# Performance work log

Measured on AMD Instinct MI355X. Metric: run time of the kernel, lower is better.

Reference implementation:

```python
import jax, jax.numpy as jnp
import numpy as np

EPS = 1e-5


def setup_inputs() -> dict:
    key = jax.random.key(0)
    ks = jax.random.split(key, 8)
    b, n, l, e = 2, 16, 1024, 512
    qd, kd, vd = 64, 64, 64
    x = jax.random.normal(ks[0], (b, n, l, e), dtype=jnp.float32)
    past_kv = jax.random.normal(ks[1], (b, n, kd, vd), dtype=jnp.float32)
    s = 1.0 / np.sqrt(e)
    Wq = jax.random.normal(ks[2], (qd, e), dtype=jnp.float32) * s
    bq = jnp.zeros((qd,), dtype=jnp.float32)
    Wk = jax.random.normal(ks[3], (kd, e), dtype=jnp.float32) * s
    bk = jnp.zeros((kd,), dtype=jnp.float32)
    Wv = jax.random.normal(ks[4], (vd, e), dtype=jnp.float32) * s
    bv = jnp.zeros((vd,), dtype=jnp.float32)
    return {"x": x, "past_kv": past_kv, "Wq": Wq, "bq": bq,
            "Wk": Wk, "bk": bk, "Wv": Wv, "bv": bv}


def reference(x, past_kv, Wq, bq, Wk, bk, Wv, bv):
    b, n, l, e = x.shape
    # QKV projections on the last axis: [b,n,l,e] -> [b,n,l,d]
    q = jnp.einsum('bnle,de->bnld', x, Wq) + bq
    k = jnp.einsum('bnle,de->bnld', x, Wk) + bk
    v = jnp.einsum('bnle,de->bnld', x, Wv) + bv
    # RetNet per-head decay: 1 - 2^(-5-h), shape [1,n,1,1,1]
    decay = 1.0 - jnp.exp2(-5.0 - jnp.arange(n, dtype=jnp.float32))
    decay = decay.reshape(1, n, 1, 1, 1)
    # decayed state + per-position outer product k_t (x) v_t -> [b,n,l,kd,vd]
    current_kv = decay * past_kv[:, :, None, :, :] + k[..., :, None] * v[..., None, :]
    # Q-weighted reduction over k_dim -> [b,n,l,vd]
    out = jnp.einsum('bnlk,bnlkv->bnlv', q, current_kv)
    # F.group_norm(out, num_groups=n): per (b, head), normalize over (l, vd)
    mean = jnp.mean(out, axis=(2, 3), keepdims=True)
    var = jnp.var(out, axis=(2, 3), keepdims=True)
    out = (out - mean) * jax.lax.rsqrt(var + EPS)
    return out, current_kv
```

## Files before the change

### kernel.cpp

```cpp
#include <hip/hip_runtime.h>


constexpr int B  = 2;
constexpr int NH = 16;
constexpr int L  = 1024;
constexpr int E  = 512;
constexpr int D  = 64;
constexpr int M  = B * NH * L;
constexpr int NQKV = 192;
constexpr int BLK = 32;
constexpr int NBLKS = M / BLK;
constexpr float EPS = 1e-5f;

using short8 = __attribute__((ext_vector_type(8))) short;
using f32x4  = __attribute__((ext_vector_type(4))) float;

__device__ __forceinline__ unsigned short f2bf(float f) {
    union { float f; unsigned int u; } x; x.f = f;
    unsigned int u = x.u;
    return (unsigned short)((u + 0x7fffu + ((u >> 16) & 1u)) >> 16);
}
__device__ __forceinline__ float bf2f(unsigned short h) {
    union { unsigned int u; float f; } x; x.u = ((unsigned int)h) << 16;
    return x.f;
}

__global__ __launch_bounds__(256) void convw_kernel(
    const float* __restrict__ Wq, const float* __restrict__ Wk,
    const float* __restrict__ Wv, unsigned short* __restrict__ Wb)
{
    int idx = blockIdx.x * 256 + threadIdx.x;
    const float* src = (idx < 8192) ? Wq : (idx < 16384) ? Wk : Wv;
    int off = idx & 8191;
    float4 v = ((const float4*)src)[off];
    Wb[(size_t)idx * 4 + 0] = f2bf(v.x);
    Wb[(size_t)idx * 4 + 1] = f2bf(v.y);
    Wb[(size_t)idx * 4 + 2] = f2bf(v.z);
    Wb[(size_t)idx * 4 + 3] = f2bf(v.w);
}

__global__ __launch_bounds__(512) void proj_mfma_kernel(
    const float* __restrict__ x, const unsigned short* __restrict__ Wb,
    const float* __restrict__ bq, const float* __restrict__ bk,
    const float* __restrict__ bv,
    unsigned short* __restrict__ qkvb)
{
    constexpr int BM = 64, BK = 64, LDP = 72;
    __shared__ unsigned short Xs[BM][LDP];
    __shared__ unsigned short Ws[NQKV][LDP];
    __shared__ float bias_s[NQKV];

    const int tid  = threadIdx.x;
    const int row0 = blockIdx.x * BM;
    if (tid < NQKV)
        bias_s[tid] = (tid < 64) ? bq[tid] : (tid < 128) ? bk[tid - 64] : bv[tid - 128];

    const int wid  = tid >> 6;
    const int lane = tid & 63;
    const int wr   = wid >> 2;
    const int wc   = wid & 3;
    const int l15  = lane & 15;
    const int lk   = (lane >> 4) * 8;

    f32x4 acc[2][3] = {};

    for (int k0 = 0; k0 < E; k0 += BK) {
        float4 xa[2];
        #pragma unroll
        for (int j = 0; j < 2; ++j) {
            int f = tid + j * 512;
            xa[j] = *(const float4*)&x[(size_t)(row0 + (f >> 4)) * E + k0 + (f & 15) * 4];
        }
        short8 wch[3];
        #pragma unroll
        for (int j = 0; j < 3; ++j) {
            int c = tid + j * 512;
            wch[j] = *(const short8*)&Wb[(size_t)(c >> 3) * E + k0 + (c & 7) * 8];
        }
        __syncthreads();
        #pragma unroll
        for (int j = 0; j < 2; ++j) {
            int f = tid + j * 512;
            unsigned short t4[4] = {f2bf(xa[j].x), f2bf(xa[j].y),
                                    f2bf(xa[j].z), f2bf(xa[j].w)};
            *(uint2*)&Xs[f >> 4][(f & 15) * 4] = *(uint2*)t4;
        }
        #pragma unroll
        for (int j = 0; j < 3; ++j) {
            int c = tid + j * 512;
            *(short8*)&Ws[c >> 3][(c & 7) * 8] = wch[j];
        }
        __syncthreads();

        #pragma unroll
        for (int kk = 0; kk < 2; ++kk) {
            short8 a[2], b[3];
            #pragma unroll
            for (int mi = 0; mi < 2; ++mi)
                a[mi] = *(const short8*)&Xs[wr * 32 + mi * 16 + l15][kk * 32 + lk];
            #pragma unroll
            for (int ni = 0; ni < 3; ++ni)
                b[ni] = *(const short8*)&Ws[wc * 48 + ni * 16 + l15][kk * 32 + lk];
            #pragma unroll
            for (int mi = 0; mi < 2; ++mi)
                #pragma unroll
                for (int ni = 0; ni < 3; ++ni)
                    acc[mi][ni] = __builtin_amdgcn_mfma_f32_16x16x32_bf16(
                        a[mi], b[ni], acc[mi][ni], 0, 0, 0);
        }
    }

    #pragma unroll
    for (int mi = 0; mi < 2; ++mi) {
        #pragma unroll
        for (int ni = 0; ni < 3; ++ni) {
            int col = wc * 48 + ni * 16 + l15;
            float bb = bias_s[col];
            #pragma unroll
            for (int j = 0; j < 4; ++j) {
                int row = wr * 32 + mi * 16 + (lane >> 4) * 4 + j;
                qkvb[(size_t)(row0 + row) * NQKV + col] = f2bf(acc[mi][ni][j] + bb);
            }
        }
    }
}

__global__ __launch_bounds__(512) void retention_kernel(
    const unsigned short* __restrict__ qkvb,
    const float* __restrict__ past_kv,
    float* __restrict__ out_pre,
    float* __restrict__ ckv,
    float* __restrict__ partials)
{
    const int blk  = blockIdx.x;
    const int bn   = blk >> 5;
    const int pos0 = (blk & 31) * BLK;
    const int h    = bn & (NH - 1);
    const int tid  = threadIdx.x;
    const float decay = 1.0f - exp2f(-5.0f - (float)h);

    __shared__ float pkv_s[64 * 64];
    __shared__ unsigned short qkv_s[BLK * NQKV];
    __shared__ float qk_s[BLK];
    __shared__ float red[16];

    const float* pkv = past_kv + (size_t)bn * 4096;
    float4 p4[2];
    #pragma unroll
    for (int j = 0; j < 2; ++j) {
        p4[j] = *(const float4*)&pkv[(tid + j * 512) * 4];
        *(float4*)&pkv_s[(tid + j * 512) * 4] = p4[j];
    }
    const unsigned short* qrow = qkvb + (size_t)(bn * L + pos0) * NQKV;
    for (int f = tid; f < 768; f += 512)
        ((uint4*)qkv_s)[f] = ((const uint4*)qrow)[f];
    __syncthreads();

    {
        int pos = tid >> 4, c = tid & 15;
        const unsigned short* qp = &qkv_s[pos * NQKV];
        float p = 0.0f;
        #pragma unroll
        for (int j = 0; j < 4; ++j)
            p = fmaf(bf2f(qp[c * 4 + j]), bf2f(qp[64 + c * 4 + j]), p);
        p += __shfl_xor(p, 1); p += __shfl_xor(p, 2);
        p += __shfl_xor(p, 4); p += __shfl_xor(p, 8);
        if (c == 0) qk_s[pos] = p;
    }

    float* co = ckv + (size_t)(bn * L + pos0) * 4096;
    const int kd0 = tid >> 4, vc = (tid & 15) * 4;
    #pragma unroll 2
    for (int pos = 0; pos < BLK; ++pos) {
        const unsigned short* ks = &qkv_s[pos * NQKV + 64];
        const unsigned short* vs = &qkv_s[pos * NQKV + 128];
        unsigned short vb[4];
        *(uint2*)vb = *(const uint2*)&vs[vc];
        float v0 = bf2f(vb[0]), v1 = bf2f(vb[1]),
              v2 = bf2f(vb[2]), v3 = bf2f(vb[3]);
        float kk0 = bf2f(ks[kd0]);
        float kk1 = bf2f(ks[kd0 + 32]);
        f32x4 r0, r1;
        r0.x = fmaf(decay, p4[0].x, kk0 * v0);
        r0.y = fmaf(decay, p4[0].y, kk0 * v1);
        r0.z = fmaf(decay, p4[0].z, kk0 * v2);
        r0.w = fmaf(decay, p4[0].w, kk0 * v3);
        r1.x = fmaf(decay, p4[1].x, kk1 * v0);
        r1.y = fmaf(decay, p4[1].y, kk1 * v1);
        r1.z = fmaf(decay, p4[1].z, kk1 * v2);
        r1.w = fmaf(decay, p4[1].w, kk1 * v3);
        __builtin_nontemporal_store(r0, (f32x4*)&co[(size_t)pos * 4096 + tid * 4]);
        __builtin_nontemporal_store(r1, (f32x4*)&co[(size_t)pos * 4096 + (tid + 512) * 4]);
    }
    __syncthreads();

    const int wave = tid >> 6, lane = tid & 63;
    const int vd = lane;
    float accs[4] = {0.0f, 0.0f, 0.0f, 0.0f};
    for (int kd = 0; kd < 64; ++kd) {
        float pv = pkv_s[kd * 64 + vd];
        #pragma unroll
        for (int pp = 0; pp < 4; ++pp)
            accs[pp] = fmaf(bf2f(qkv_s[(wave + pp * 8) * NQKV + kd]), pv, accs[pp]);
    }
    float s1 = 0.0f, s2 = 0.0f;
    #pragma unroll
    for (int pp = 0; pp < 4; ++pp) {
        int pos = wave + pp * 8;
        float o = fmaf(decay, accs[pp],
                       qk_s[pos] * bf2f(qkv_s[pos * NQKV + 128 + vd]));
        out_pre[(size_t)(bn * L + pos0 + pos) * D + vd] = o;
        s1 += o; s2 += o * o;
    }

    #pragma unroll
    for (int off = 32; off; off >>= 1) {
        s1 += __shfl_down(s1, off);
        s2 += __shfl_down(s2, off);
    }
    if (lane == 0) { red[wave * 2] = s1; red[wave * 2 + 1] = s2; }
    __syncthreads();
    if (tid == 0) {
        float a = 0.0f, b2 = 0.0f;
        #pragma unroll
        for (int w = 0; w < 8; ++w) { a += red[w * 2]; b2 += red[w * 2 + 1]; }
        partials[(size_t)blk * 2]     = a;
        partials[(size_t)blk * 2 + 1] = b2;
    }
}

__global__ __launch_bounds__(64) void group_reduce_kernel(
    const float* __restrict__ partials, float* __restrict__ stats)
{
    const int g   = blockIdx.x;
    const int tid = threadIdx.x;
    float s1 = 0.0f, s2 = 0.0f;
    if (tid < 32) {
        s1 = partials[(size_t)(g * 32 + tid) * 2];
        s2 = partials[(size_t)(g * 32 + tid) * 2 + 1];
    }
    #pragma unroll
    for (int off = 16; off; off >>= 1) {
        s1 += __shfl_down(s1, off);
        s2 += __shfl_down(s2, off);
    }
    if (tid == 0) {
        const float cnt = (float)(L * D);
        float mean = s1 / cnt;
        float var  = s2 / cnt - mean * mean;
        stats[g * 2]     = mean;
        stats[g * 2 + 1] = rsqrtf(var + EPS);
    }
}

__global__ __launch_bounds__(256) void normalize_kernel(
    float* __restrict__ out, const float* __restrict__ stats)
{
    int idx = blockIdx.x * 256 + threadIdx.x;
    int g = idx >> 14;
    float mean = stats[g * 2];
    float rstd = stats[g * 2 + 1];
    f32x4 v = *((const f32x4*)out + idx);
    v.x = (v.x - mean) * rstd; v.y = (v.y - mean) * rstd;
    v.z = (v.z - mean) * rstd; v.w = (v.w - mean) * rstd;
    __builtin_nontemporal_store(v, (f32x4*)out + idx);
}

extern "C" void kernel_launch(void* const* d_in, const int* in_sizes, int n_in,
                              void* d_out, int out_size, void* d_ws, size_t ws_size,
                              hipStream_t stream)
{
    const float* x       = (const float*)d_in[0];
    const float* past_kv = (const float*)d_in[1];
    const float* Wq      = (const float*)d_in[2];
    const float* bq      = (const float*)d_in[3];
    const float* Wk      = (const float*)d_in[4];
    const float* bk      = (const float*)d_in[5];
    const float* Wv      = (const float*)d_in[6];
    const float* bv      = (const float*)d_in[7];

    float* out = (float*)d_out;
    float* ckv = out + (size_t)M * 64;

    unsigned short* Wb   = (unsigned short*)d_ws;
    unsigned short* qkvb = Wb + (size_t)NQKV * E;
    float* partials = (float*)(qkvb + (size_t)M * NQKV);
    float* stats    = partials + (size_t)NBLKS * 2;

    convw_kernel<<<96, 256, 0, stream>>>(Wq, Wk, Wv, Wb);
    proj_mfma_kernel<<<M / 64, 512, 0, stream>>>(x, Wb, bq, bk, bv, qkvb);
    retention_kernel<<<NBLKS, 512, 0, stream>>>(qkvb, past_kv, out, ckv, partials);
    group_reduce_kernel<<<32, 64, 0, stream>>>(partials, stats);
    normalize_kernel<<<(M * 16) / 256, 256, 0, stream>>>(out, stats);
}
```

Baseline: 137.9 us.

## Fuse retention output into projection kernel and split off state store kernel

The q·past_kv reduction, the q·k term and the group-norm partial sums now run in the projection kernel, reusing the bf16 QKV tile already in shared memory. past_kv is staged as bf16 in the freed LDS. A separate lean kernel writes the large current_kv tensor with 256 threads per block. The pre-norm output goes to a workspace buffer so normalize reads from it instead of working in place. The intent is to separate the store-bound state write from the compute work and drop the extra shared-memory staging. The cost is a longer projection kernel and reduced precision for past_kv in the output path.

```diff
diff --git a/kernel.cpp b/kernel.cpp
--- a/kernel.cpp
+++ b/kernel.cpp
@@ -8,8 +8,10 @@
 constexpr int D  = 64;
 constexpr int M  = B * NH * L;
 constexpr int NQKV = 192;
-constexpr int BLK = 32;
-constexpr int NBLKS = M / BLK;
+constexpr int PBLK = 64;
+constexpr int NPBLKS = M / PBLK;
+constexpr int SBLK = 32;
+constexpr int NSBLKS = M / SBLK;
 constexpr float EPS = 1e-5f;
 
 using short8 = __attribute__((ext_vector_type(8))) short;
@@ -39,19 +41,31 @@
     Wb[(size_t)idx * 4 + 3] = f2bf(v.w);
 }
 
-__global__ __launch_bounds__(512) void proj_mfma_kernel(
+__global__ __launch_bounds__(512) void proj_out_kernel(
     const float* __restrict__ x, const unsigned short* __restrict__ Wb,
     const float* __restrict__ bq, const float* __restrict__ bk,
     const float* __restrict__ bv,
-    unsigned short* __restrict__ qkvb)
-{
-    constexpr int BM = 64, BK = 64, LDP = 72;
-    __shared__ unsigned short Xs[BM][LDP];
+    const float* __restrict__ past_kv,
+    unsigned short* __restrict__ qkvb,
+    float* __restrict__ out_pre,
+    float* __restrict__ partials)
+{
+    constexpr int BK = 64, LDP = 72, QSP = 200;
+    __shared__ unsigned short Xs[PBLK][LDP];
     __shared__ unsigned short Ws[NQKV][LDP];
     __shared__ float bias_s[NQKV];
-
+    __shared__ float qk_s[PBLK];
+    __shared__ float red[16];
+    auto pkv_s = (unsigned short*)&Xs[0][0];
+    auto qs    = (unsigned short(*)[QSP])&Ws[0][0];
+
+    const int blk  = blockIdx.x;
+    const int bn   = blk >> 4;
+    const int row0 = blk * PBLK;
+    const int h    = bn & (NH - 1);
     const int tid  = threadIdx.x;
-    const int row0 = blockIdx.x * BM;
+    const float decay = 1.0f - exp2f(-5.0f - (float)h);
+
     if (tid < NQKV)
         bias_s[tid] = (tid < 64) ? bq[tid] : (tid < 128) ? bk[tid - 64] : bv[tid - 128];
 
@@ -109,6 +123,7 @@
                         a[mi], b[ni], acc[mi][ni], 0, 0, 0);
         }
     }
+    __syncthreads();
 
     #pragma unroll
     for (int mi = 0; mi < 2; ++mi) {
@@ -119,113 +134,122 @@
             #pragma unroll
             for (int j = 0; j < 4; ++j) {
                 int row = wr * 32 + mi * 16 + (lane >> 4) * 4 + j;
-                qkvb[(size_t)(row0 + row) * NQKV + col] = f2bf(acc[mi][ni][j] + bb);
+                unsigned short val = f2bf(acc[mi][ni][j] + bb);
+                qkvb[(size_t)(row0 + row) * NQKV + col] = val;
+                qs[row][col] = val;
             }
         }
     }
-}
-
-__global__ __launch_bounds__(512) void retention_kernel(
+    const float* pkv = past_kv + (size_t)bn * 4096;
+    #pragma unroll
+    for (int j = 0; j < 2; ++j) {
+        float4 pv = *(const float4*)&pkv[(tid + j * 512) * 4];
+        unsigned short t4[4] = {f2bf(pv.x), f2bf(pv.y), f2bf(pv.z), f2bf(pv.w)};
+        *(uint2*)&pkv_s[(tid + j * 512) * 4] = *(uint2*)t4;
+    }
+    __syncthreads();
+
+    {
+        int pos = tid >> 3, c = tid & 7;
+        float p = 0.0f;
+        #pragma unroll
+        for (int j = 0; j < 8; ++j)
+            p = fmaf(bf2f(qs[pos][c * 8 + j]), bf2f(qs[pos][64 + c * 8 + j]), p);
+        p += __shfl_xor(p, 1); p += __shfl_xor(p, 2); p += __shfl_xor(p, 4);
+        if (c == 0) qk_s[pos] = p;
+    }
+    __syncthreads();
+
+    float accs[8] = {};
+    #pragma unroll
+    for (int half = 0; half < 2; ++half) {
+        for (int kt = 0; kt < 8; ++kt) {
+            short8 q8[4];
+            #pragma unroll
+            for (int pi = 0; pi < 4; ++pi)
+                q8[pi] = *(const short8*)&qs[wid + (half * 4 + pi) * 8][kt * 8];
+            #pragma unroll
+            for (int j = 0; j < 8; ++j) {
+                float pv = bf2f(pkv_s[(kt * 8 + j) * 64 + lane]);
+                #pragma unroll
+                for (int pi = 0; pi < 4; ++pi)
+                    accs[half * 4 + pi] = fmaf(
+                        bf2f((unsigned short)q8[pi][j]), pv, accs[half * 4 + pi]);
+            }
+        }
+    }
+    float s1 = 0.0f, s2 = 0.0f;
+    #pragma unroll
+    for (int pp = 0; pp < 8; ++pp) {
+        int pos = wid + pp * 8;
+        float o = fmaf(decay, accs[pp], qk_s[pos] * bf2f(qs[pos][128 + lane]));
+        __builtin_nontemporal_store(o, &out_pre[(size_t)(row0 + pos) * D + lane]);
+        s1 += o; s2 += o * o;
+    }
+
+    #pragma unroll
+    for (int off = 32; off; off >>= 1) {
+        s1 += __shfl_down(s1, off);
+        s2 += __shfl_down(s2, off);
+    }
+    if (lane == 0) { red[wid * 2] = s1; red[wid * 2 + 1] = s2; }
+    __syncthreads();
+    if (tid == 0) {
+        float a = 0.0f, b2 = 0.0f;
+        #pragma unroll
+        for (int w = 0; w < 8; ++w) { a += red[w * 2]; b2 += red[w * 2 + 1]; }
+        partials[(size_t)blk * 2]     = a;
+        partials[(size_t)blk * 2 + 1] = b2;
+    }
+}
+
+__global__ __launch_bounds__(256) void store_kernel(
     const unsigned short* __restrict__ qkvb,
     const float* __restrict__ past_kv,
-    float* __restrict__ out_pre,
-    float* __restrict__ ckv,
-    float* __restrict__ partials)
-{
+    float* __restrict__ ckv)
+{
+    __shared__ unsigned short qkv_s[SBLK * NQKV];
+
     const int blk  = blockIdx.x;
     const int bn   = blk >> 5;
-    const int pos0 = (blk & 31) * BLK;
+    const int pos0 = (blk & 31) * SBLK;
     const int h    = bn & (NH - 1);
     const int tid  = threadIdx.x;
     const float decay = 1.0f - exp2f(-5.0f - (float)h);
 
-    __shared__ float pkv_s[64 * 64];
-    __shared__ unsigned short qkv_s[BLK * NQKV];
-    __shared__ float qk_s[BLK];
-    __shared__ float red[16];
+    const unsigned short* qrow = qkvb + (size_t)(bn * L + pos0) * NQKV;
+    #pragma unroll
+    for (int j = 0; j < 3; ++j)
+        ((uint4*)qkv_s)[tid + j * 256] = ((const uint4*)qrow)[tid + j * 256];
 
     const float* pkv = past_kv + (size_t)bn * 4096;
-    float4 p4[2];
-    #pragma unroll
-    for (int j = 0; j < 2; ++j) {
-        p4[j] = *(const float4*)&pkv[(tid + j * 512) * 4];
-        *(float4*)&pkv_s[(tid + j * 512) * 4] = p4[j];
-    }
-    const unsigned short* qrow = qkvb + (size_t)(bn * L + pos0) * NQKV;
-    for (int f = tid; f < 768; f += 512)
-        ((uint4*)qkv_s)[f] = ((const uint4*)qrow)[f];
-    __syncthreads();
-
-    {
-        int pos = tid >> 4, c = tid & 15;
-        const unsigned short* qp = &qkv_s[pos * NQKV];
-        float p = 0.0f;
-        #pragma unroll
-        for (int j = 0; j < 4; ++j)
-            p = fmaf(bf2f(qp[c * 4 + j]), bf2f(qp[64 + c * 4 + j]), p);
-        p += __shfl_xor(p, 1); p += __shfl_xor(p, 2);
-        p += __shfl_xor(p, 4); p += __shfl_xor(p, 8);
-        if (c == 0) qk_s[pos] = p;
-    }
+    float4 p4[4];
+    #pragma unroll
+    for (int j = 0; j < 4; ++j)
+        p4[j] = *(const float4*)&pkv[(tid + j * 256) * 4];
+    __syncthreads();
 
     float* co = ckv + (size_t)(bn * L + pos0) * 4096;
-    const int kd0 = tid >> 4, vc = (tid & 15) * 4;
+    const int vc = (tid & 15) * 4;
     #pragma unroll 2
-    for (int pos = 0; pos < BLK; ++pos) {
+    for (int pos = 0; pos < SBLK; ++pos) {
         const unsigned short* ks = &qkv_s[pos * NQKV + 64];
         const unsigned short* vs = &qkv_s[pos * NQKV + 128];
         unsigned short vb[4];
         *(uint2*)vb = *(const uint2*)&vs[vc];
         float v0 = bf2f(vb[0]), v1 = bf2f(vb[1]),
               v2 = bf2f(vb[2]), v3 = bf2f(vb[3]);
-        float kk0 = bf2f(ks[kd0]);
-        float kk1 = bf2f(ks[kd0 + 32]);
-        f32x4 r0, r1;
-        r0.x = fmaf(decay, p4[0].x, kk0 * v0);
-        r0.y = fmaf(decay, p4[0].y, kk0 * v1);
-        r0.z = fmaf(decay, p4[0].z, kk0 * v2);
-        r0.w = fmaf(decay, p4[0].w, kk0 * v3);
-        r1.x = fmaf(decay, p4[1].x, kk1 * v0);
-        r1.y = fmaf(decay, p4[1].y, kk1 * v1);
-        r1.z = fmaf(decay, p4[1].z, kk1 * v2);
-        r1.w = fmaf(decay, p4[1].w, kk1 * v3);
-        __builtin_nontemporal_store(r0, (f32x4*)&co[(size_t)pos * 4096 + tid * 4]);
-        __builtin_nontemporal_store(r1, (f32x4*)&co[(size_t)pos * 4096 + (tid + 512) * 4]);
-    }
-    __syncthreads();
-
-    const int wave = tid >> 6, lane = tid & 63;
-    const int vd = lane;
-    float accs[4] = {0.0f, 0.0f, 0.0f, 0.0f};
-    for (int kd = 0; kd < 64; ++kd) {
-        float pv = pkv_s[kd * 64 + vd];
-        #pragma unroll
-        for (int pp = 0; pp < 4; ++pp)
-            accs[pp] = fmaf(bf2f(qkv_s[(wave + pp * 8) * NQKV + kd]), pv, accs[pp]);
-    }
-    float s1 = 0.0f, s2 = 0.0f;
-    #pragma unroll
-    for (int pp = 0; pp < 4; ++pp) {
-        int pos = wave + pp * 8;
-        float o = fmaf(decay, accs[pp],
-                       qk_s[pos] * bf2f(qkv_s[pos * NQKV + 128 + vd]));
-        out_pre[(size_t)(bn * L + pos0 + pos) * D + vd] = o;
-        s1 += o; s2 += o * o;
-    }
-
-    #pragma unroll
-    for (int off = 32; off; off >>= 1) {
-        s1 += __shfl_down(s1, off);
-        s2 += __shfl_down(s2, off);
-    }
-    if (lane == 0) { red[wave * 2] = s1; red[wave * 2 + 1] = s2; }
-    __syncthreads();
-    if (tid == 0) {
-        float a = 0.0f, b2 = 0.0f;
-        #pragma unroll
-        for (int w = 0; w < 8; ++w) { a += red[w * 2]; b2 += red[w * 2 + 1]; }
-        partials[(size_t)blk * 2]     = a;
-        partials[(size_t)blk * 2 + 1] = b2;
+        #pragma unroll
+        for (int j = 0; j < 4; ++j) {
+            int f = tid + j * 256;
+            float kk = bf2f(ks[f >> 4]);
+            f32x4 r;
+            r.x = fmaf(decay, p4[j].x, kk * v0);
+            r.y = fmaf(decay, p4[j].y, kk * v1);
+            r.z = fmaf(decay, p4[j].z, kk * v2);
+            r.w = fmaf(decay, p4[j].w, kk * v3);
+            __builtin_nontemporal_store(r, (f32x4*)&co[(size_t)pos * 4096 + f * 4]);
+        }
     }
 }
 
@@ -235,12 +259,12 @@
     const int g   = blockIdx.x;
     const int tid = threadIdx.x;
     float s1 = 0.0f, s2 = 0.0f;
-    if (tid < 32) {
-        s1 = partials[(size_t)(g * 32 + tid) * 2];
-        s2 = partials[(size_t)(g * 32 + tid) * 2 + 1];
-    }
-    #pragma unroll
-    for (int off = 16; off; off >>= 1) {
+    if (tid < 16) {
+        s1 = partials[(size_t)(g * 16 + tid) * 2];
+        s2 = partials[(size_t)(g * 16 + tid) * 2 + 1];
+    }
+    #pragma unroll
+    for (int off = 8; off; off >>= 1) {
         s1 += __shfl_down(s1, off);
         s2 += __shfl_down(s2, off);
     }
@@ -254,13 +278,14 @@
 }
 
 __global__ __launch_bounds__(256) void normalize_kernel(
-    float* __restrict__ out, const float* __restrict__ stats)
+    const float* __restrict__ out_pre, float* __restrict__ out,
+    const float* __restrict__ stats)
 {
     int idx = blockIdx.x * 256 + threadIdx.x;
     int g = idx >> 14;
     float mean = stats[g * 2];
     float rstd = stats[g * 2 + 1];
-    f32x4 v = *((const f32x4*)out + idx);
+    f32x4 v = *((const f32x4*)out_pre + idx);
     v.x = (v.x - mean) * rstd; v.y = (v.y - mean) * rstd;
     v.z = (v.z - mean) * rstd; v.w = (v.w - mean) * rstd;
     __builtin_nontemporal_store(v, (f32x4*)out + idx);
@@ -285,11 +310,13 @@
     unsigned short* Wb   = (unsigned short*)d_ws;
     unsigned short* qkvb = Wb + (size_t)NQKV * E;
     float* partials = (float*)(qkvb + (size_t)M * NQKV);
-    float* stats    = partials + (size_t)NBLKS * 2;
+    float* stats    = partials + (size_t)NPBLKS * 2;
+    float* out_pre  = stats + 64;
 
     convw_kernel<<<96, 256, 0, stream>>>(Wq, Wk, Wv, Wb);
-    proj_mfma_kernel<<<M / 64, 512, 0, stream>>>(x, Wb, bq, bk, bv, qkvb);
-    retention_kernel<<<NBLKS, 512, 0, stream>>>(qkvb, past_kv, out, ckv, partials);
+    proj_out_kernel<<<NPBLKS, 512, 0, stream>>>(x, Wb, bq, bk, bv, past_kv,
+                                                qkvb, out_pre, partials);
+    store_kernel<<<NSBLKS, 256, 0, stream>>>(qkvb, past_kv, ckv);
     group_reduce_kernel<<<32, 64, 0, stream>>>(partials, stats);
-    normalize_kernel<<<(M * 16) / 256, 256, 0, stream>>>(out, stats);
-}
+    normalize_kernel<<<(M * 16) / 256, 256, 0, stream>>>(out_pre, out, stats);
+}
```

Result: slower. 157.3 us (+14.1%).

## Shrink retention blocks to 8 positions and swizzle block order across XCDs

Applied to the files above, without the earlier changes.

The retention kernel now processes 8 positions per 256-thread block instead of 32 per 512-thread block, giving four times as many blocks. It drops the past_kv shared-memory copy and reads past_kv straight from global/L2 in the q·past_kv reduction. Block indices in both the projection and retention kernels are permuted, (bid&7)*stride + bid>>3, so that consecutive workgroups, which are spread across the 8 XCDs, land on contiguous rows. The group reduction is updated to sum 128 partials per group. The intent is better occupancy and L2 locality for the large ckv write stream, at the cost of more block launches and more redundant past_kv loads.

```diff
diff --git a/kernel.cpp b/kernel.cpp
--- a/kernel.cpp
+++ b/kernel.cpp
@@ -8,8 +8,8 @@
 constexpr int D  = 64;
 constexpr int M  = B * NH * L;
 constexpr int NQKV = 192;
-constexpr int BLK = 32;
-constexpr int NBLKS = M / BLK;
+constexpr int SBLK = 8;
+constexpr int NSBLKS = M / SBLK;
 constexpr float EPS = 1e-5f;
 
 using short8 = __attribute__((ext_vector_type(8))) short;
@@ -51,7 +51,8 @@
     __shared__ float bias_s[NQKV];
 
     const int tid  = threadIdx.x;
-    const int row0 = blockIdx.x * BM;
+    const int blk  = (blockIdx.x & 7) * 64 + (blockIdx.x >> 3);
+    const int row0 = blk * BM;
     if (tid < NQKV)
         bias_s[tid] = (tid < 64) ? bq[tid] : (tid < 128) ? bk[tid - 64] : bv[tid - 128];
 
@@ -125,94 +126,84 @@
     }
 }
 
-__global__ __launch_bounds__(512) void retention_kernel(
+__global__ __launch_bounds__(256) void store_out_kernel(
     const unsigned short* __restrict__ qkvb,
     const float* __restrict__ past_kv,
-    float* __restrict__ out_pre,
+    float* __restrict__ out,
     float* __restrict__ ckv,
     float* __restrict__ partials)
 {
-    const int blk  = blockIdx.x;
-    const int bn   = blk >> 5;
-    const int pos0 = (blk & 31) * BLK;
+    __shared__ unsigned short qkv_s[SBLK * NQKV];
+    __shared__ float qk_s[SBLK];
+    __shared__ float red[8];
+
+    const int blk  = (blockIdx.x & 7) * 512 + (blockIdx.x >> 3);
+    const int bn   = blk >> 7;
+    const int pos0 = (blk & 127) * SBLK;
     const int h    = bn & (NH - 1);
     const int tid  = threadIdx.x;
     const float decay = 1.0f - exp2f(-5.0f - (float)h);
 
-    __shared__ float pkv_s[64 * 64];
-    __shared__ unsigned short qkv_s[BLK * NQKV];
-    __shared__ float qk_s[BLK];
-    __shared__ float red[16];
+    const unsigned short* qrow = qkvb + (size_t)(bn * L + pos0) * NQKV;
+    if (tid < 192) ((uint4*)qkv_s)[tid] = ((const uint4*)qrow)[tid];
 
     const float* pkv = past_kv + (size_t)bn * 4096;
-    float4 p4[2];
-    #pragma unroll
-    for (int j = 0; j < 2; ++j) {
-        p4[j] = *(const float4*)&pkv[(tid + j * 512) * 4];
-        *(float4*)&pkv_s[(tid + j * 512) * 4] = p4[j];
-    }
-    const unsigned short* qrow = qkvb + (size_t)(bn * L + pos0) * NQKV;
-    for (int f = tid; f < 768; f += 512)
-        ((uint4*)qkv_s)[f] = ((const uint4*)qrow)[f];
+    float4 p4[4];
+    #pragma unroll
+    for (int j = 0; j < 4; ++j)
+        p4[j] = *(const float4*)&pkv[(tid + j * 256) * 4];
     __syncthreads();
 
-    {
-        int pos = tid >> 4, c = tid & 15;
+    if (tid < 64) {
+        int pos = tid >> 3, c = tid & 7;
         const unsigned short* qp = &qkv_s[pos * NQKV];
         float p = 0.0f;
         #pragma unroll
-        for (int j = 0; j < 4; ++j)
-            p = fmaf(bf2f(qp[c * 4 + j]), bf2f(qp[64 + c * 4 + j]), p);
-        p += __shfl_xor(p, 1); p += __shfl_xor(p, 2);
-        p += __shfl_xor(p, 4); p += __shfl_xor(p, 8);
+        for (int j = 0; j < 8; ++j)
+            p = fmaf(bf2f(qp[c * 8 + j]), bf2f(qp[64 + c * 8 + j]), p);
+        p += __shfl_xor(p, 1); p += __shfl_xor(p, 2); p += __shfl_xor(p, 4);
         if (c == 0) qk_s[pos] = p;
     }
 
     float* co = ckv + (size_t)(bn * L + pos0) * 4096;
     const int kd0 = tid >> 4, vc = (tid & 15) * 4;
     #pragma unroll 2
-    for (int pos = 0; pos < BLK; ++pos) {
+    for (int pos = 0; pos < SBLK; ++pos) {
         const unsigned short* ks = &qkv_s[pos * NQKV + 64];
         const unsigned short* vs = &qkv_s[pos * NQKV + 128];
         unsigned short vb[4];
         *(uint2*)vb = *(const uint2*)&vs[vc];
         float v0 = bf2f(vb[0]), v1 = bf2f(vb[1]),
               v2 = bf2f(vb[2]), v3 = bf2f(vb[3]);
-        float kk0 = bf2f(ks[kd0]);
-        float kk1 = bf2f(ks[kd0 + 32]);
-        f32x4 r0, r1;
-        r0.x = fmaf(decay, p4[0].x, kk0 * v0);
-        r0.y = fmaf(decay, p4[0].y, kk0 * v1);
-        r0.z = fmaf(decay, p4[0].z, kk0 * v2);
-        r0.w = fmaf(decay, p4[0].w, kk0 * v3);
-        r1.x = fmaf(decay, p4[1].x, kk1 * v0);
-        r1.y = fmaf(decay, p4[1].y, kk1 * v1);
-        r1.z = fmaf(decay, p4[1].z, kk1 * v2);
-        r1.w = fmaf(decay, p4[1].w, kk1 * v3);
-        __builtin_nontemporal_store(r0, (f32x4*)&co[(size_t)pos * 4096 + tid * 4]);
-        __builtin_nontemporal_store(r1, (f32x4*)&co[(size_t)pos * 4096 + (tid + 512) * 4]);
+        #pragma unroll
+        for (int j = 0; j < 4; ++j) {
+            float kk = bf2f(ks[kd0 + j * 16]);
+            f32x4 r;
+            r.x = fmaf(decay, p4[j].x, kk * v0);
+            r.y = fmaf(decay, p4[j].y, kk * v1);
+            r.z = fmaf(decay, p4[j].z, kk * v2);
+            r.w = fmaf(decay, p4[j].w, kk * v3);
+            __builtin_nontemporal_store(
+                r, (f32x4*)&co[(size_t)pos * 4096 + (tid + j * 256) * 4]);
+        }
     }
     __syncthreads();
 
     const int wave = tid >> 6, lane = tid & 63;
-    const int vd = lane;
-    float accs[4] = {0.0f, 0.0f, 0.0f, 0.0f};
+    float a0 = 0.0f, a1 = 0.0f;
+    const unsigned short* q0 = &qkv_s[wave * NQKV];
+    const unsigned short* q1 = &qkv_s[(wave + 4) * NQKV];
     for (int kd = 0; kd < 64; ++kd) {
-        float pv = pkv_s[kd * 64 + vd];
-        #pragma unroll
-        for (int pp = 0; pp < 4; ++pp)
-            accs[pp] = fmaf(bf2f(qkv_s[(wave + pp * 8) * NQKV + kd]), pv, accs[pp]);
-    }
-    float s1 = 0.0f, s2 = 0.0f;
-    #pragma unroll
-    for (int pp = 0; pp < 4; ++pp) {
-        int pos = wave + pp * 8;
-        float o = fmaf(decay, accs[pp],
-                       qk_s[pos] * bf2f(qkv_s[pos * NQKV + 128 + vd]));
-        out_pre[(size_t)(bn * L + pos0 + pos) * D + vd] = o;
-        s1 += o; s2 += o * o;
-    }
-
+        float pv = pkv[kd * 64 + lane];
+        a0 = fmaf(bf2f(q0[kd]), pv, a0);
+        a1 = fmaf(bf2f(q1[kd]), pv, a1);
+    }
+    float o0 = fmaf(decay, a0, qk_s[wave]     * bf2f(q0[128 + lane]));
+    float o1 = fmaf(decay, a1, qk_s[wave + 4] * bf2f(q1[128 + lane]));
+    out[(size_t)(bn * L + pos0 + wave) * D + lane]     = o0;
+    out[(size_t)(bn * L + pos0 + wave + 4) * D + lane] = o1;
+
+    float s1 = o0 + o1, s2 = o0 * o0 + o1 * o1;
     #pragma unroll
     for (int off = 32; off; off >>= 1) {
         s1 += __shfl_down(s1, off);
@@ -223,7 +214,7 @@
     if (tid == 0) {
         float a = 0.0f, b2 = 0.0f;
         #pragma unroll
-        for (int w = 0; w < 8; ++w) { a += red[w * 2]; b2 += red[w * 2 + 1]; }
+        for (int w = 0; w < 4; ++w) { a += red[w * 2]; b2 += red[w * 2 + 1]; }
         partials[(size_t)blk * 2]     = a;
         partials[(size_t)blk * 2 + 1] = b2;
     }
@@ -234,13 +225,12 @@
 {
     const int g   = blockIdx.x;
     const int tid = threadIdx.x;
-    float s1 = 0.0f, s2 = 0.0f;
-    if (tid < 32) {
-        s1 = partials[(size_t)(g * 32 + tid) * 2];
-        s2 = partials[(size_t)(g * 32 + tid) * 2 + 1];
-    }
-    #pragma unroll
-    for (int off = 16; off; off >>= 1) {
+    float s1 = partials[(size_t)(g * 128 + tid) * 2]
+             + partials[(size_t)(g * 128 + 64 + tid) * 2];
+    float s2 = partials[(size_t)(g * 128 + tid) * 2 + 1]
+             + partials[(size_t)(g * 128 + 64 + tid) * 2 + 1];
+    #pragma unroll
+    for (int off = 32; off; off >>= 1) {
         s1 += __shfl_down(s1, off);
         s2 += __shfl_down(s2, off);
     }
@@ -285,11 +275,11 @@
     unsigned short* Wb   = (unsigned short*)d_ws;
     unsigned short* qkvb = Wb + (size_t)NQKV * E;
     float* partials = (float*)(qkvb + (size_t)M * NQKV);
-    float* stats    = partials + (size_t)NBLKS * 2;
+    float* stats    = partials + (size_t)NSBLKS * 2;
 
     convw_kernel<<<96, 256, 0, stream>>>(Wq, Wk, Wv, Wb);
     proj_mfma_kernel<<<M / 64, 512, 0, stream>>>(x, Wb, bq, bk, bv, qkvb);
-    retention_kernel<<<NBLKS, 512, 0, stream>>>(qkvb, past_kv, out, ckv, partials);
+    store_out_kernel<<<NSBLKS, 256, 0, stream>>>(qkvb, past_kv, out, ckv, partials);
     group_reduce_kernel<<<32, 64, 0, stream>>>(partials, stats);
     normalize_kernel<<<(M * 16) / 256, 256, 0, stream>>>(out, stats);
 }
```

Result: faster. 134.8 us (-2.3%).
